# Optimization experiments

Hardware: AMD Instinct MI355X
Metric: run time of the kernel (lower is better)

Reference implementation:

```python
import jax, jax.numpy as jnp
import numpy as np

HIDDEN = 1024
NUM_HEAD = 16
HEAD_DIM = HIDDEN // NUM_HEAD


def setup_inputs() -> dict:
    key = jax.random.key(0)
    ks = jax.random.split(key, 9)
    B, S = 1, 4096
    scale = 1.0 / np.sqrt(HIDDEN)
    inp = {
        "x": jax.random.normal(ks[0], (B, S, HIDDEN), dtype=jnp.float32),
        "wq": jax.random.normal(ks[1], (HIDDEN, HIDDEN), dtype=jnp.float32) * scale,
        "bq": jnp.zeros((HIDDEN,), dtype=jnp.float32),
        "wk": jax.random.normal(ks[2], (HIDDEN, HIDDEN), dtype=jnp.float32) * scale,
        "bk": jnp.zeros((HIDDEN,), dtype=jnp.float32),
        "wv": jax.random.normal(ks[3], (HIDDEN, HIDDEN), dtype=jnp.float32) * scale,
        "bv": jnp.zeros((HIDDEN,), dtype=jnp.float32),
        "wo": jax.random.normal(ks[4], (HIDDEN, HIDDEN), dtype=jnp.float32) * scale,
        "bo": jnp.zeros((HIDDEN,), dtype=jnp.float32),
    }
    return inp


def reference(x, wq, bq, wk, bk, wv, bv, wo, bo):
    B, S, _ = x.shape
    # QKV projections (torch Linear: x @ W.T + b)
    def split_heads(t):
        return t.reshape(B, S, NUM_HEAD, HEAD_DIM).transpose(0, 2, 1, 3)  # [B,H,S,D]
    q = split_heads(x @ wq.T + bq)
    k = split_heads(x @ wk.T + bk)
    v = split_heads(x @ wv.T + bv)
    # scaled dot-product scores: [B,H,S,S]
    scores = jnp.einsum('bhsd,bhtd->bhst', q, k) / jnp.sqrt(jnp.float32(HEAD_DIM))
    # faithful double softmax over the key axis (no mask; dropout = eval identity)
    attn = jax.nn.softmax(scores, axis=-1)
    attn = jax.nn.softmax(attn, axis=-1)
    out = jnp.einsum('bhst,bhtd->bhsd', attn, v)  # [B,H,S,D]
    out = out.transpose(0, 2, 1, 3).reshape(B, S, HIDDEN)
    return out @ wo.T + bo
```

## Files before the change

kernel.cpp:

```cpp
#include <hip/hip_runtime.h>
#include <hip/hip_bf16.h>
#include <stdint.h>

#define S 4096
#define HID 1024
#define NH 16
#define DH 64

typedef __attribute__((ext_vector_type(8))) short short8;
typedef __attribute__((ext_vector_type(2))) float f32x2;
typedef __attribute__((ext_vector_type(4))) float f32x4;
typedef __attribute__((ext_vector_type(16))) float f32x16;
typedef __attribute__((ext_vector_type(4))) unsigned int u32x4;

#define VMCNT8 asm volatile("s_waitcnt vmcnt(8)" ::: "memory")
#define VMCNT0 asm volatile("s_waitcnt vmcnt(0)" ::: "memory")
#define LGKM0  asm volatile("s_waitcnt lgkmcnt(0)" ::: "memory")

__device__ __forceinline__ unsigned short f2bf(float f) {
  unsigned int u = __builtin_bit_cast(unsigned int, f);
  u += 0x7FFF + ((u >> 16) & 1);
  return (unsigned short)(u >> 16);
}
__device__ __forceinline__ unsigned int pktrunc(float lo, float hi) {
  return __builtin_amdgcn_perm(__builtin_bit_cast(unsigned int, hi),
                               __builtin_bit_cast(unsigned int, lo), 0x07060302u);
}
__device__ __forceinline__ void gload16(const unsigned short* g, unsigned short* l) {
  __builtin_amdgcn_global_load_lds((const __attribute__((address_space(1))) unsigned int*)g,
                                   (__attribute__((address_space(3))) unsigned int*)l, 16, 0, 0);
}

__global__ __launch_bounds__(256) void cast_kernel(
    const float* __restrict__ x,  const float* __restrict__ wq,
    const float* __restrict__ wk, const float* __restrict__ wv,
    const float* __restrict__ wo,
    unsigned short* __restrict__ xb,  unsigned short* __restrict__ wqb,
    unsigned short* __restrict__ wkb, unsigned short* __restrict__ wvb,
    unsigned short* __restrict__ wob)
{
  int y = blockIdx.y;
  const float* src; unsigned short* dst; int n;
  if      (y == 0) { src = x;  dst = xb;  n = S * HID; }
  else if (y == 1) { src = wq; dst = wqb; n = HID * HID; }
  else if (y == 2) { src = wk; dst = wkb; n = HID * HID; }
  else if (y == 3) { src = wv; dst = wvb; n = HID * HID; }
  else             { src = wo; dst = wob; n = HID * HID; }
  int i = (blockIdx.x * 256 + threadIdx.x) * 4;
  if (i < n) {
    float4 v = *reinterpret_cast<const float4*>(src + i);
    ushort4 o;
    o.x = f2bf(v.x); o.y = f2bf(v.y); o.z = f2bf(v.z); o.w = f2bf(v.w);
    *reinterpret_cast<ushort4*>(dst + i) = o;
  }
}

__device__ __forceinline__ void gemm128(
    const unsigned short* __restrict__ A, const unsigned short* __restrict__ W,
    unsigned short* As, unsigned short* Bs, f32x4 acc[4][4], int row0, int col0)
{
  const int tid = threadIdx.x;
  const int wave = tid >> 6, lane = tid & 63, quad = lane >> 4, l16 = lane & 15;
  const int wr = (wave >> 1) * 64, wc = (wave & 1) * 64;
  const int srow = lane >> 2, sseg = lane & 3;
  const f32x4 z = {0.f, 0.f, 0.f, 0.f};
  #pragma unroll
  for (int i = 0; i < 4; i++)
    #pragma unroll
    for (int j = 0; j < 4; j++) acc[i][j] = z;

  for (int k0 = 0; k0 < HID; k0 += 32) {
    __syncthreads();
    #pragma unroll
    for (int c = 0; c < 2; c++) {
      const int rbase = c * 64 + wave * 16;
      gload16(A + (size_t)(row0 + rbase + srow) * HID + k0 + sseg * 8, As + rbase * 32);
      gload16(W + (size_t)(col0 + rbase + srow) * HID + k0 + sseg * 8, Bs + rbase * 32);
    }
    __syncthreads();

    short8 af[4], bfr[4];
    #pragma unroll
    for (int i = 0; i < 4; i++)
      af[i] = *reinterpret_cast<const short8*>(As + (wr + i * 16 + l16) * 32 + quad * 8);
    #pragma unroll
    for (int j = 0; j < 4; j++)
      bfr[j] = *reinterpret_cast<const short8*>(Bs + (wc + j * 16 + l16) * 32 + quad * 8);
    #pragma unroll
    for (int i = 0; i < 4; i++)
      #pragma unroll
      for (int j = 0; j < 4; j++)
        acc[i][j] = __builtin_amdgcn_mfma_f32_16x16x32_bf16(af[i], bfr[j], acc[i][j], 0, 0, 0);
  }
}

__global__ __launch_bounds__(256) void qkv_gemm_kernel(
    const unsigned short* __restrict__ X,
    const unsigned short* __restrict__ Wq, const unsigned short* __restrict__ Wk,
    const unsigned short* __restrict__ Wv,
    const float* __restrict__ bq, const float* __restrict__ bk, const float* __restrict__ bv,
    unsigned short* __restrict__ Qo, unsigned short* __restrict__ K2o, unsigned short* __restrict__ Vbo)
{
  __shared__ unsigned short As[128 * 32];
  __shared__ unsigned short Bs[128 * 32];
  const int zsel = blockIdx.z;
  const unsigned short* W = (zsel == 0) ? Wq : (zsel == 1) ? Wk : Wv;
  const float* bias        = (zsel == 0) ? bq : (zsel == 1) ? bk : bv;
  const int row0 = blockIdx.x * 128, col0 = blockIdx.y * 128;
  f32x4 acc[4][4];
  gemm128(X, W, As, Bs, acc, row0, col0);

  const int tid = threadIdx.x;
  const int wave = tid >> 6, lane = tid & 63, quad = lane >> 4, l16 = lane & 15;
  const int wr = (wave >> 1) * 64, wc = (wave & 1) * 64;

  if (zsel == 0) {
    const float osc = 0.18033688011112042f;
    #pragma unroll
    for (int j = 0; j < 4; j++) {
      int n = col0 + wc + j * 16 + l16;
      float bb = bias[n];
      int h = n >> 6, d = n & 63;
      #pragma unroll
      for (int i = 0; i < 4; i++)
        #pragma unroll
        for (int rr = 0; rr < 4; rr++) {
          int s = row0 + wr + i * 16 + quad * 4 + rr;
          Qo[(size_t)(h * S + s) * DH + d] = f2bf((acc[i][j][rr] + bb) * osc);
        }
    }
  } else if (zsel == 1) {
    #pragma unroll
    for (int j = 0; j < 4; j++) {
      int n = col0 + wc + j * 16 + l16;
      float bb = bias[n];
      int h = n >> 6, dh = n & 63;
      int c = dh >> 4, hfk = (dh >> 3) & 1, j8 = dh & 7;
      #pragma unroll
      for (int i = 0; i < 4; i++)
        #pragma unroll
        for (int rr = 0; rr < 4; rr++) {
          int s = row0 + wr + i * 16 + quad * 4 + rr;
          int g = s >> 5, l32k = s & 31;
          K2o[((size_t)((h * 128 + g) * 4 + c) * 64 + hfk * 32 + l32k) * 8 + j8] =
              f2bf(acc[i][j][rr] + bb);
        }
    }
  } else {
    #pragma unroll
    for (int j = 0; j < 4; j++) {
      int n = col0 + wc + j * 16 + l16;
      float bb = bias[n];
      int h = n >> 6, dh = n & 63;
      int ng = dh >> 5, l32v = dh & 31;
      int hf_v = quad & 1, jj0 = (quad >> 1) * 4;
      #pragma unroll
      for (int i = 0; i < 4; i++) {
        int gt = (row0 + wr + i * 16) >> 5;
        int grp = i & 1;
        ushort4 pv;
        pv.x = f2bf(acc[i][j][0] + bb); pv.y = f2bf(acc[i][j][1] + bb);
        pv.z = f2bf(acc[i][j][2] + bb); pv.w = f2bf(acc[i][j][3] + bb);
        *reinterpret_cast<ushort4*>(
            Vbo + ((size_t)(((h * 128 + gt) * 2 + grp) * 2 + ng) * 64 + hf_v * 32 + l32v) * 8 + jj0) = pv;
      }
    }
  }
}

__global__ __launch_bounds__(256) void out_gemm_kernel(
    const unsigned short* __restrict__ A, const unsigned short* __restrict__ W,
    const float* __restrict__ be, float* __restrict__ dst)
{
  __shared__ unsigned short As[128 * 32];
  __shared__ unsigned short Bs[128 * 32];
  const int row0 = blockIdx.x * 128, col0 = blockIdx.y * 128;
  f32x4 acc[4][4];
  gemm128(A, W, As, Bs, acc, row0, col0);

  const int tid = threadIdx.x;
  const int wave = tid >> 6, lane = tid & 63, quad = lane >> 4, l16 = lane & 15;
  const int wr = (wave >> 1) * 64, wc = (wave & 1) * 64;
  #pragma unroll
  for (int j = 0; j < 4; j++) {
    int n = col0 + wc + j * 16 + l16;
    float bb = be[n];
    #pragma unroll
    for (int i = 0; i < 4; i++)
      #pragma unroll
      for (int rr = 0; rr < 4; rr++) {
        int s = row0 + wr + i * 16 + quad * 4 + rr;
        dst[(size_t)s * HID + n] = acc[i][j][rr] + bb;
      }
  }
}

__global__ __launch_bounds__(256) void vsum_kernel(
    const unsigned short* __restrict__ Vb, float* __restrict__ VsumP)
{
  __shared__ float red[256];
  const int p = blockIdx.x, h = blockIdx.y, tid = threadIdx.x;
  const int d = tid & 63, chunk = tid >> 6;
  const int ng = d >> 5, l32 = d & 31;
  float s = 0.f;
  for (int m = 0; m < 4; m++) {
    int gt = p * 16 + chunk * 4 + m;
    #pragma unroll
    for (int grp = 0; grp < 2; grp++)
      #pragma unroll
      for (int hf = 0; hf < 2; hf++) {
        uint4 u = *reinterpret_cast<const uint4*>(
            Vb + ((size_t)(((h * 128 + gt) * 2 + grp) * 2 + ng) * 64 + hf * 32 + l32) * 8);
        const unsigned int w[4] = {u.x, u.y, u.z, u.w};
        #pragma unroll
        for (int q = 0; q < 4; q++) {
          s += __builtin_bit_cast(float, w[q] << 16);
          s += __builtin_bit_cast(float, w[q] & 0xFFFF0000u);
        }
      }
  }
  red[tid] = s;
  __syncthreads();
  if (tid < 64)
    VsumP[p * 1024 + h * 64 + tid] = red[tid] + red[64 + tid] + red[128 + tid] + red[192 + tid];
}

__global__ __launch_bounds__(256) void biasfold_kernel(
    const float* __restrict__ VsumP, const float* __restrict__ wo,
    const float* __restrict__ bo, float* __restrict__ be)
{
  const int n = blockIdx.x * 4 + (threadIdx.x >> 6);
  const int l = threadIdx.x & 63;
  float acc = 0.f;
  #pragma unroll
  for (int i = 0; i < 16; i++) {
    float vs = 0.f;
    #pragma unroll
    for (int p = 0; p < 8; p++) vs += VsumP[p * 1024 + l + 64 * i];
    acc += vs * wo[(size_t)n * HID + l + 64 * i];
  }
  #pragma unroll
  for (int off = 32; off >= 1; off >>= 1) acc += __shfl_xor(acc, off);
  if (l == 0) be[n] = bo[n] + acc * (1.f / 4097.f);
}

struct AttnState {
  short8 qf[2][4];
  f32x16 Oa[2][2];
  f32x16 zacc;
  f32x2  zp[2];
};

__device__ __forceinline__ void loadregs(
    const unsigned short* kb, const unsigned short* vb,
    short8 (&kf)[4], short8 (&vf)[4])
{
  #pragma unroll
  for (int c = 0; c < 4; c++)
    kf[c] = *reinterpret_cast<const short8*>(kb + c * 512);
  #pragma unroll
  for (int w = 0; w < 4; w++)
    vf[w] = *reinterpret_cast<const short8*>(vb + w * 512);
}

__device__ __forceinline__ void attn_compute(
    const short8 (&kf)[4], const short8 (&vfr)[4], AttnState& st)
{
  #pragma unroll
  for (int qh = 0; qh < 2; qh++) {
    f32x16 acc = __builtin_amdgcn_mfma_f32_32x32x16_bf16(kf[0], st.qf[qh][0], st.zacc, 0, 0, 0);
    #pragma unroll
    for (int c = 1; c < 4; c++)
      acc = __builtin_amdgcn_mfma_f32_32x32x16_bf16(kf[c], st.qf[qh][c], acc, 0, 0, 0);

    unsigned int D[8];
    #pragma unroll
    for (int m = 0; m < 8; m++) {
      float t0 = __builtin_amdgcn_exp2f(acc[2 * m]);
      float t1 = __builtin_amdgcn_exp2f(acc[2 * m + 1]);
      f32x2 t = {t0, t1};
      st.zp[qh] += t;
      D[m] = pktrunc(t0, t1);
    }
    u32x4 dv0 = {D[0], D[1], D[2], D[3]};
    u32x4 dv1 = {D[4], D[5], D[6], D[7]};
    short8 A0 = __builtin_bit_cast(short8, dv0);
    short8 A1 = __builtin_bit_cast(short8, dv1);

    st.Oa[qh][0] = __builtin_amdgcn_mfma_f32_32x32x16_bf16(A0, vfr[0], st.Oa[qh][0], 0, 0, 0);
    st.Oa[qh][1] = __builtin_amdgcn_mfma_f32_32x32x16_bf16(A0, vfr[1], st.Oa[qh][1], 0, 0, 0);
    st.Oa[qh][0] = __builtin_amdgcn_mfma_f32_32x32x16_bf16(A1, vfr[2], st.Oa[qh][0], 0, 0, 0);
    st.Oa[qh][1] = __builtin_amdgcn_mfma_f32_32x32x16_bf16(A1, vfr[3], st.Oa[qh][1], 0, 0, 0);
  }
}

__device__ __forceinline__ void stage_tile(
    const unsigned short* gK, const unsigned short* gV,
    unsigned short* lK, unsigned short* lV)
{
  #pragma unroll
  for (int i = 0; i < 4; i++) gload16(gK + i * 512, lK + i * 512);
  #pragma unroll
  for (int i = 0; i < 4; i++) gload16(gV + i * 512, lV + i * 512);
}

__global__ __launch_bounds__(256, 2) void attn_kernel(
    const unsigned short* __restrict__ Q, const unsigned short* __restrict__ K2,
    const unsigned short* __restrict__ Vb, unsigned short* __restrict__ OUT)
{
  __shared__ unsigned short T[4][2][2][2048];
  __shared__ float Zl[256];
  float* Ored = reinterpret_cast<float*>(&T[0][0][0][0]);

  const int lin = blockIdx.y * 64 + blockIdx.x;
  const int xcd = lin & 7, idx = lin >> 3;
  const int h = xcd * 2 + (idx >> 6);
  const int q0 = (idx & 63) * 64;

  const int tid = threadIdx.x;
  const int wave = tid >> 6, lane = tid & 63, hf = lane >> 5, l32 = lane & 31;

  AttnState st;
  #pragma unroll
  for (int qh = 0; qh < 2; qh++) {
    const unsigned short* qrow = Q + (size_t)(h * S + q0 + qh * 32 + l32) * DH;
    #pragma unroll
    for (int c = 0; c < 4; c++)
      st.qf[qh][c] = *reinterpret_cast<const short8*>(qrow + c * 16 + hf * 8);
  }
  #pragma unroll
  for (int r = 0; r < 16; r++) {
    st.zacc[r] = 0.f;
    st.Oa[0][0][r] = 0.f; st.Oa[0][1][r] = 0.f;
    st.Oa[1][0][r] = 0.f; st.Oa[1][1][r] = 0.f;
  }
  st.zp[0] = (f32x2){0.f, 0.f};
  st.zp[1] = (f32x2){0.f, 0.f};

  const unsigned short* Kb  = K2 + (size_t)h * 128 * 2048;
  const unsigned short* Vbb = Vb + (size_t)h * 128 * 2048;

  const unsigned short* gK = Kb  + (size_t)wave * 2048 + (size_t)lane * 8;
  const unsigned short* gV = Vbb + (size_t)wave * 2048 + (size_t)lane * 8;
  unsigned short* lK0 = &T[wave][0][0][0];
  unsigned short* lV0 = &T[wave][0][1][0];
  unsigned short* lK1 = &T[wave][1][0][0];
  unsigned short* lV1 = &T[wave][1][1][0];
  const unsigned short* kb0 = &T[wave][0][0][0] + lane * 8;
  const unsigned short* vb0 = &T[wave][0][1][0] + lane * 8;
  const unsigned short* kb1 = &T[wave][1][0][0] + lane * 8;
  const unsigned short* vb1 = &T[wave][1][1][0] + lane * 8;
  const ptrdiff_t STR = 4 * 2048;

  short8 kA[4], vA[4], kB[4], vB[4];

  stage_tile(gK, gV, lK0, lV0); gK += STR; gV += STR;
  VMCNT0;
  loadregs(kb0, vb0, kA, vA);
  stage_tile(gK, gV, lK1, lV1); gK += STR; gV += STR;
  LGKM0;

  for (int p = 0; p < 15; p++) {
    stage_tile(gK, gV, lK0, lV0); gK += STR; gV += STR;
    VMCNT8;
    loadregs(kb1, vb1, kB, vB);
    attn_compute(kA, vA, st);
    LGKM0;
    stage_tile(gK, gV, lK1, lV1); gK += STR; gV += STR;
    VMCNT8;
    loadregs(kb0, vb0, kA, vA);
    attn_compute(kB, vB, st);
    LGKM0;
  }
  VMCNT0;
  loadregs(kb1, vb1, kB, vB);
  attn_compute(kA, vA, st);
  attn_compute(kB, vB, st);

  __syncthreads();
  {
    float za = st.zp[0][0] + st.zp[0][1];
    float zb = st.zp[1][0] + st.zp[1][1];
    za += __shfl_xor(za, 32);
    zb += __shfl_xor(zb, 32);
    if (hf == 0) {
      Zl[wave * 64 + l32]      = za;
      Zl[wave * 64 + 32 + l32] = zb;
    }
    float* Ow = Ored + wave * 4096;
    #pragma unroll
    for (int qh = 0; qh < 2; qh++)
      #pragma unroll
      for (int ng = 0; ng < 2; ng++)
        #pragma unroll
        for (int r = 0; r < 16; r++) {
          const int row = (r & 3) + 8 * (r >> 2) + 4 * hf;
          Ow[(qh * 32 + row) * 64 + ng * 32 + l32] = st.Oa[qh][ng][r];
        }
  }
  __syncthreads();
  {
    const int q = tid >> 2, d0 = (tid & 3) * 16;
    const float* O0 = Ored + q * 64 + d0;
    f32x4 s0 = *reinterpret_cast<const f32x4*>(O0);
    f32x4 s1 = *reinterpret_cast<const f32x4*>(O0 + 4);
    f32x4 s2 = *reinterpret_cast<const f32x4*>(O0 + 8);
    f32x4 s3 = *reinterpret_cast<const f32x4*>(O0 + 12);
    #pragma unroll
    for (int w = 1; w < 4; w++) {
      const float* Ow = Ored + w * 4096 + q * 64 + d0;
      s0 += *reinterpret_cast<const f32x4*>(Ow);
      s1 += *reinterpret_cast<const f32x4*>(Ow + 4);
      s2 += *reinterpret_cast<const f32x4*>(Ow + 8);
      s3 += *reinterpret_cast<const f32x4*>(Ow + 12);
    }
    const float zt = Zl[q] + Zl[64 + q] + Zl[128 + q] + Zl[192 + q];
    const float rz = 1.f / (zt * 4097.f);
    unsigned short* op = OUT + (size_t)(q0 + q) * HID + h * DH + d0;
    ushort4 u;
    u.x = f2bf(s0[0] * rz); u.y = f2bf(s0[1] * rz);
    u.z = f2bf(s0[2] * rz); u.w = f2bf(s0[3] * rz);
    *reinterpret_cast<ushort4*>(op) = u;
    u.x = f2bf(s1[0] * rz); u.y = f2bf(s1[1] * rz);
    u.z = f2bf(s1[2] * rz); u.w = f2bf(s1[3] * rz);
    *reinterpret_cast<ushort4*>(op + 4) = u;
    u.x = f2bf(s2[0] * rz); u.y = f2bf(s2[1] * rz);
    u.z = f2bf(s2[2] * rz); u.w = f2bf(s2[3] * rz);
    *reinterpret_cast<ushort4*>(op + 8) = u;
    u.x = f2bf(s3[0] * rz); u.y = f2bf(s3[1] * rz);
    u.z = f2bf(s3[2] * rz); u.w = f2bf(s3[3] * rz);
    *reinterpret_cast<ushort4*>(op + 12) = u;
  }
}

extern "C" void kernel_launch(void* const* d_in, const int* in_sizes, int n_in,
                              void* d_out, int out_size, void* d_ws, size_t ws_size,
                              hipStream_t stream) {
  const float* x  = (const float*)d_in[0];
  const float* wq = (const float*)d_in[1];
  const float* bq = (const float*)d_in[2];
  const float* wk = (const float*)d_in[3];
  const float* bk = (const float*)d_in[4];
  const float* wv = (const float*)d_in[5];
  const float* bv = (const float*)d_in[6];
  const float* wo = (const float*)d_in[7];
  const float* bo = (const float*)d_in[8];
  float* out = (float*)d_out;

  char* ws = (char*)d_ws;
  unsigned short* xb  = (unsigned short*)(ws);
  unsigned short* wqb = (unsigned short*)(ws + (8u  << 20));
  unsigned short* wkb = (unsigned short*)(ws + (10u << 20));
  unsigned short* wvb = (unsigned short*)(ws + (12u << 20));
  unsigned short* wob = (unsigned short*)(ws + (14u << 20));
  unsigned short* qw  = (unsigned short*)(ws + (16u << 20));
  unsigned short* k2  = (unsigned short*)(ws + (24u << 20));
  unsigned short* vb  = (unsigned short*)(ws + (32u << 20));
  float* vsump        = (float*)(ws + (40u << 20));
  float* be           = (float*)(ws + (40u << 20) + 65536);
  unsigned short* aw  = xb;

  cast_kernel<<<dim3(4096, 5), 256, 0, stream>>>(x, wq, wk, wv, wo, xb, wqb, wkb, wvb, wob);
  qkv_gemm_kernel<<<dim3(32, 8, 3), 256, 0, stream>>>(xb, wqb, wkb, wvb, bq, bk, bv, qw, k2, vb);
  vsum_kernel<<<dim3(8, 16), 256, 0, stream>>>(vb, vsump);
  biasfold_kernel<<<dim3(256), 256, 0, stream>>>(vsump, wo, bo, be);
  attn_kernel<<<dim3(64, 16), 256, 0, stream>>>(qw, k2, vb, aw);
  out_gemm_kernel<<<dim3(32, 8, 1), 256, 0, stream>>>(aw, wob, be, out);
}
```

Measured before the change: 241.6 us.

## Single-buffer attention K/V staging to raise occupancy to four blocks per CU

Replaces the double-buffered LDS staging and the double register set (kA/kB) with a single buffer and register set, and raises the launch bound from 2 to 4 blocks per CU. The zero accumulator moves out of persistent state into a local constant, and the final cross-wave reduction becomes a two-stage accumulate so it fits in the halved LDS. The aim is to hide latency through more resident waves instead of explicit prefetch. In exchange, each iteration now waits on vmcnt(0) before reading LDS, so global-load latency is exposed within a wave, and the tighter register budget may cause spills.

```diff
diff --git a/kernel.cpp b/kernel.cpp
--- a/kernel.cpp
+++ b/kernel.cpp
@@ -13,7 +13,6 @@
 typedef __attribute__((ext_vector_type(16))) float f32x16;
 typedef __attribute__((ext_vector_type(4))) unsigned int u32x4;
 
-#define VMCNT8 asm volatile("s_waitcnt vmcnt(8)" ::: "memory")
 #define VMCNT0 asm volatile("s_waitcnt vmcnt(0)" ::: "memory")
 #define LGKM0  asm volatile("s_waitcnt lgkmcnt(0)" ::: "memory")
 
@@ -247,7 +246,6 @@
 struct AttnState {
   short8 qf[2][4];
   f32x16 Oa[2][2];
-  f32x16 zacc;
   f32x2  zp[2];
 };
 
@@ -266,9 +264,12 @@
 __device__ __forceinline__ void attn_compute(
     const short8 (&kf)[4], const short8 (&vfr)[4], AttnState& st)
 {
+  f32x16 zacc;
+  #pragma unroll
+  for (int r = 0; r < 16; r++) zacc[r] = 0.f;
   #pragma unroll
   for (int qh = 0; qh < 2; qh++) {
-    f32x16 acc = __builtin_amdgcn_mfma_f32_32x32x16_bf16(kf[0], st.qf[qh][0], st.zacc, 0, 0, 0);
+    f32x16 acc = __builtin_amdgcn_mfma_f32_32x32x16_bf16(kf[0], st.qf[qh][0], zacc, 0, 0, 0);
     #pragma unroll
     for (int c = 1; c < 4; c++)
       acc = __builtin_amdgcn_mfma_f32_32x32x16_bf16(kf[c], st.qf[qh][c], acc, 0, 0, 0);
@@ -304,13 +305,13 @@
   for (int i = 0; i < 4; i++) gload16(gV + i * 512, lV + i * 512);
 }
 
-__global__ __launch_bounds__(256, 2) void attn_kernel(
+__global__ __launch_bounds__(256, 4) void attn_kernel(
     const unsigned short* __restrict__ Q, const unsigned short* __restrict__ K2,
     const unsigned short* __restrict__ Vb, unsigned short* __restrict__ OUT)
 {
-  __shared__ unsigned short T[4][2][2][2048];
+  __shared__ unsigned short T[4][2][2048];
   __shared__ float Zl[256];
-  float* Ored = reinterpret_cast<float*>(&T[0][0][0][0]);
+  float* Ored = reinterpret_cast<float*>(&T[0][0][0]);
 
   const int lin = blockIdx.y * 64 + blockIdx.x;
   const int xcd = lin & 7, idx = lin >> 3;
@@ -330,7 +331,6 @@
   }
   #pragma unroll
   for (int r = 0; r < 16; r++) {
-    st.zacc[r] = 0.f;
     st.Oa[0][0][r] = 0.f; st.Oa[0][1][r] = 0.f;
     st.Oa[1][0][r] = 0.f; st.Oa[1][1][r] = 0.f;
   }
@@ -342,40 +342,27 @@
 
   const unsigned short* gK = Kb  + (size_t)wave * 2048 + (size_t)lane * 8;
   const unsigned short* gV = Vbb + (size_t)wave * 2048 + (size_t)lane * 8;
-  unsigned short* lK0 = &T[wave][0][0][0];
-  unsigned short* lV0 = &T[wave][0][1][0];
-  unsigned short* lK1 = &T[wave][1][0][0];
-  unsigned short* lV1 = &T[wave][1][1][0];
-  const unsigned short* kb0 = &T[wave][0][0][0] + lane * 8;
-  const unsigned short* vb0 = &T[wave][0][1][0] + lane * 8;
-  const unsigned short* kb1 = &T[wave][1][0][0] + lane * 8;
-  const unsigned short* vb1 = &T[wave][1][1][0] + lane * 8;
+  unsigned short* lK = &T[wave][0][0];
+  unsigned short* lV = &T[wave][1][0];
+  const unsigned short* kb = &T[wave][0][0] + lane * 8;
+  const unsigned short* vb = &T[wave][1][0] + lane * 8;
   const ptrdiff_t STR = 4 * 2048;
 
-  short8 kA[4], vA[4], kB[4], vB[4];
-
-  stage_tile(gK, gV, lK0, lV0); gK += STR; gV += STR;
+  short8 kf[4], vf[4];
+
+  stage_tile(gK, gV, lK, lV); gK += STR; gV += STR;
   VMCNT0;
-  loadregs(kb0, vb0, kA, vA);
-  stage_tile(gK, gV, lK1, lV1); gK += STR; gV += STR;
+  loadregs(kb, vb, kf, vf);
   LGKM0;
 
-  for (int p = 0; p < 15; p++) {
-    stage_tile(gK, gV, lK0, lV0); gK += STR; gV += STR;
-    VMCNT8;
-    loadregs(kb1, vb1, kB, vB);
-    attn_compute(kA, vA, st);
+  for (int t = 0; t < 31; t++) {
+    stage_tile(gK, gV, lK, lV); gK += STR; gV += STR;
+    attn_compute(kf, vf, st);
+    VMCNT0;
+    loadregs(kb, vb, kf, vf);
     LGKM0;
-    stage_tile(gK, gV, lK1, lV1); gK += STR; gV += STR;
-    VMCNT8;
-    loadregs(kb0, vb0, kA, vA);
-    attn_compute(kB, vB, st);
-    LGKM0;
-  }
-  VMCNT0;
-  loadregs(kb1, vb1, kB, vB);
-  attn_compute(kA, vA, st);
-  attn_compute(kB, vB, st);
+  }
+  attn_compute(kf, vf, st);
 
   __syncthreads();
   {
@@ -387,6 +374,21 @@
       Zl[wave * 64 + l32]      = za;
       Zl[wave * 64 + 32 + l32] = zb;
     }
+    if (wave >= 2) {
+      float* Ow = Ored + (wave - 2) * 4096;
+      #pragma unroll
+      for (int qh = 0; qh < 2; qh++)
+        #pragma unroll
+        for (int ng = 0; ng < 2; ng++)
+          #pragma unroll
+          for (int r = 0; r < 16; r++) {
+            const int row = (r & 3) + 8 * (r >> 2) + 4 * hf;
+            Ow[(qh * 32 + row) * 64 + ng * 32 + l32] = st.Oa[qh][ng][r];
+          }
+    }
+  }
+  __syncthreads();
+  if (wave < 2) {
     float* Ow = Ored + wave * 4096;
     #pragma unroll
     for (int qh = 0; qh < 2; qh++)
@@ -395,25 +397,19 @@
         #pragma unroll
         for (int r = 0; r < 16; r++) {
           const int row = (r & 3) + 8 * (r >> 2) + 4 * hf;
-          Ow[(qh * 32 + row) * 64 + ng * 32 + l32] = st.Oa[qh][ng][r];
+          const int ix = (qh * 32 + row) * 64 + ng * 32 + l32;
+          Ow[ix] += st.Oa[qh][ng][r];
         }
   }
   __syncthreads();
   {
     const int q = tid >> 2, d0 = (tid & 3) * 16;
     const float* O0 = Ored + q * 64 + d0;
-    f32x4 s0 = *reinterpret_cast<const f32x4*>(O0);
-    f32x4 s1 = *reinterpret_cast<const f32x4*>(O0 + 4);
-    f32x4 s2 = *reinterpret_cast<const f32x4*>(O0 + 8);
-    f32x4 s3 = *reinterpret_cast<const f32x4*>(O0 + 12);
-    #pragma unroll
-    for (int w = 1; w < 4; w++) {
-      const float* Ow = Ored + w * 4096 + q * 64 + d0;
-      s0 += *reinterpret_cast<const f32x4*>(Ow);
-      s1 += *reinterpret_cast<const f32x4*>(Ow + 4);
-      s2 += *reinterpret_cast<const f32x4*>(Ow + 8);
-      s3 += *reinterpret_cast<const f32x4*>(Ow + 12);
-    }
+    const float* O1 = Ored + 4096 + q * 64 + d0;
+    f32x4 s0 = *reinterpret_cast<const f32x4*>(O0)      + *reinterpret_cast<const f32x4*>(O1);
+    f32x4 s1 = *reinterpret_cast<const f32x4*>(O0 + 4)  + *reinterpret_cast<const f32x4*>(O1 + 4);
+    f32x4 s2 = *reinterpret_cast<const f32x4*>(O0 + 8)  + *reinterpret_cast<const f32x4*>(O1 + 8);
+    f32x4 s3 = *reinterpret_cast<const f32x4*>(O0 + 12) + *reinterpret_cast<const f32x4*>(O1 + 12);
     const float zt = Zl[q] + Zl[64 + q] + Zl[128 + q] + Zl[192 + q];
     const float rz = 1.f / (zt * 4097.f);
     unsigned short* op = OUT + (size_t)(q0 + q) * HID + h * DH + d0;
```

After: 319.0 us. 1.32x slower.
